# Optimization experiments

Measured on AMD Instinct MI355X. Metric: run time of the kernel, lower is better.

Reference implementation:

```python
import jax, jax.numpy as jnp
import numpy as np

MODEL_DIM = 1024
NUM_HEADS = 16
HEAD_DIM = MODEL_DIM // NUM_HEADS
WINDOW = 4


def local_mask(seq_len):
    i = jnp.arange(seq_len)
    return jnp.abs(i[:, None] - i[None, :]) <= WINDOW  # [S,S] bool


def setup_inputs() -> dict:
    key = jax.random.key(0)
    ks = jax.random.split(key, 9)
    d = MODEL_DIM
    s = 0.02
    return {
        "x": jax.random.normal(ks[0], (4, 2048, d), dtype=jnp.float32),
        "Wq": jax.random.normal(ks[1], (d, d), dtype=jnp.float32) * s,
        "bq": jnp.zeros((d,), dtype=jnp.float32),
        "Wk": jax.random.normal(ks[2], (d, d), dtype=jnp.float32) * s,
        "bk": jnp.zeros((d,), dtype=jnp.float32),
        "Wv": jax.random.normal(ks[3], (d, d), dtype=jnp.float32) * s,
        "bv": jnp.zeros((d,), dtype=jnp.float32),
        "Wo": jax.random.normal(ks[4], (d, d), dtype=jnp.float32) * s,
        "bo": jnp.zeros((d,), dtype=jnp.float32),
    }


def reference(x, Wq, bq, Wk, bk, Wv, bv, Wo, bo):
    B, S, D = x.shape
    H, Hd = NUM_HEADS, HEAD_DIM
    # linear projections (torch Linear: x @ W.T + b; here W stored pre-transposed)
    q = (x @ Wq + bq).reshape(B, S, H, Hd).transpose(0, 2, 1, 3)  # [B,H,S,Hd]
    k = (x @ Wk + bk).reshape(B, S, H, Hd).transpose(0, 2, 1, 3)
    v = (x @ Wv + bv).reshape(B, S, H, Hd).transpose(0, 2, 1, 3)
    scores = jnp.einsum("bhqd,bhkd->bhqk", q, k) / jnp.sqrt(jnp.float32(Hd))
    mask = local_mask(S)[None, None]  # [1,1,S,S]
    scores = jnp.where(mask, scores, -jnp.inf)
    weights = jax.nn.softmax(scores, axis=-1)  # [B,H,S,S]
    out = jnp.einsum("bhqk,bhkd->bhqd", weights, v)
    out = out.transpose(0, 2, 1, 3).reshape(B, S, D)
    out = out @ Wo + bo
    return (out, weights)
```

## Files before the change

kernel.cpp:

```cpp
#include <hip/hip_runtime.h>


typedef __attribute__((ext_vector_type(8))) short short8;
typedef __attribute__((ext_vector_type(4))) float f32x4;

#define B_    4
#define S_    2048
#define D_    1024
#define H_    16
#define HD_   64
#define WIN_  4
#define NROW  (B_ * S_)
#define OUT0_ELEMS  ((size_t)B_ * S_ * D_)
#define TOTAL_CH (67108864ull)
#define Z0_CH 37748736ull
#define Z1_CH 16777216ull
#define ZA_BASE (Z0_CH + Z1_CH)

__device__ __forceinline__ unsigned short f2bf(float f) {
  unsigned int u = __float_as_uint(f);
  u += 0x7fffu + ((u >> 16) & 1u);
  return (unsigned short)(u >> 16);
}
__device__ __forceinline__ float bf2f(unsigned short u) {
  return __uint_as_float(((unsigned int)u) << 16);
}

__device__ __forceinline__ void zstore(f32x4* __restrict__ woutv, size_t g) {
  int row = (int)(g >> 9);
  int f = (int)(g & 511);
  int s = row & (S_ - 1);
  int f0 = (s > WIN_) ? ((s - WIN_) >> 2) : 0;
  int hi = (s + WIN_ < S_ - 1) ? (s + WIN_) : (S_ - 1);
  int f1 = hi >> 2;
  if (f < f0 || f > f1) {
    f32x4 z = {0.f, 0.f, 0.f, 0.f};
    __builtin_nontemporal_store(z, woutv + g);
  }
}

__global__ __launch_bounds__(256) void xconv_k(const float* __restrict__ x,
                                               unsigned short* __restrict__ o) {
  int i = blockIdx.x * 256 + threadIdx.x;
  float4 f = reinterpret_cast<const float4*>(x)[i];
  ushort4 u;
  u.x = f2bf(f.x); u.y = f2bf(f.y); u.z = f2bf(f.z); u.w = f2bf(f.w);
  reinterpret_cast<ushort4*>(o)[i] = u;
}

__global__ __launch_bounds__(256) void wconv_k(const float* __restrict__ W0,
                                               const float* __restrict__ W1,
                                               const float* __restrict__ W2,
                                               const float* __restrict__ W3,
                                               unsigned short* __restrict__ out) {
  __shared__ float t[32][33];
  const float* Ws[4] = {W0, W1, W2, W3};
  const float* W = Ws[blockIdx.z];
  unsigned short* o = out + (size_t)blockIdx.z * D_ * D_;
  int tx = threadIdx.x;
  int ty = threadIdx.y;
  int n0 = blockIdx.x * 32, k0 = blockIdx.y * 32;
#pragma unroll
  for (int i = 0; i < 4; ++i)
    t[ty + 8 * i][tx] = W[(size_t)(k0 + ty + 8 * i) * D_ + (n0 + tx)];
  __syncthreads();
#pragma unroll
  for (int i = 0; i < 4; ++i)
    o[(size_t)(n0 + ty + 8 * i) * D_ + (k0 + tx)] = f2bf(t[tx][ty + 8 * i]);
}

#define GLD16(g, l)                                                            \
  __builtin_amdgcn_global_load_lds(                                            \
      (const __attribute__((address_space(1))) unsigned int*)(g),              \
      (__attribute__((address_space(3))) unsigned int*)(l), 16, 0, 0)

__global__ __launch_bounds__(256) void gemm_qkv_k(
    const unsigned short* __restrict__ A, const unsigned short* __restrict__ Wt,
    const float* __restrict__ bq, const float* __restrict__ bk,
    const float* __restrict__ bv, unsigned short* __restrict__ Qb,
    unsigned short* __restrict__ Kb, unsigned short* __restrict__ Vb,
    float* __restrict__ wout) {
  __shared__ unsigned short As[128 * 32];
  __shared__ unsigned short Bs[128 * 32];
  const int b = blockIdx.x;
  const int g8 = b >> 3, o = b & 7;

  if ((g8 & 3) == 3) {
    const int fb = (g8 >> 2) * 8 + o;
    const unsigned int t0 = fb * 256u + threadIdx.x;
    f32x4* woutv = (f32x4*)wout;
    for (int it = 0; it < 288; ++it)
      zstore(woutv, (size_t)it * 131072u + t0);
    return;
  }

  const int gg = g8 - (g8 >> 2);
  const int row0 = (o * 8 + (gg & 7)) * 128;
  const int col0 = (gg >> 3) * 128;

  const int tid = threadIdx.x;
  const int lane = tid & 63;
  const int wid = tid >> 6;
  const int wm = wid >> 1, wn = wid & 1;

  f32x4 acc[4][4] = {};
  const int frow = lane & 15;
  const int koff = (lane >> 4) << 3;

  for (int kt = 0; kt < 32; ++kt) {
#pragma unroll
    for (int i = 0; i < 2; ++i) {
      int c = tid + (i << 8);
      int r = c >> 2;
      int kk = (c & 3) << 3;
      GLD16(A + (size_t)(row0 + r) * D_ + (kt << 5) + kk, (char*)As + c * 16);
      GLD16(Wt + (size_t)(col0 + r) * D_ + (kt << 5) + kk, (char*)Bs + c * 16);
    }
    __syncthreads();
    short8 af[4], bfr[4];
#pragma unroll
    for (int mi = 0; mi < 4; ++mi)
      af[mi] = *reinterpret_cast<const short8*>(
          &As[(wm * 64 + mi * 16 + frow) * 32 + koff]);
#pragma unroll
    for (int ni = 0; ni < 4; ++ni)
      bfr[ni] = *reinterpret_cast<const short8*>(
          &Bs[(wn * 64 + ni * 16 + frow) * 32 + koff]);
#pragma unroll
    for (int mi = 0; mi < 4; ++mi)
#pragma unroll
      for (int ni = 0; ni < 4; ++ni)
        acc[mi][ni] = __builtin_amdgcn_mfma_f32_16x16x32_bf16(
            af[mi], bfr[ni], acc[mi][ni], 0, 0, 0);
    __syncthreads();
  }

#pragma unroll
  for (int mi = 0; mi < 4; ++mi) {
#pragma unroll
    for (int ni = 0; ni < 4; ++ni) {
#pragma unroll
      for (int r = 0; r < 4; ++r) {
        int gr = row0 + wm * 64 + mi * 16 + ((lane >> 4) << 2) + r;
        int gc = col0 + wn * 64 + ni * 16 + (lane & 15);
        int z = gc >> 10;
        int ci = gc & 1023;
        float bias = (z == 0) ? bq[ci] : (z == 1) ? bk[ci] : bv[ci];
        unsigned short* outp = (z == 0) ? Qb : (z == 1) ? Kb : Vb;
        int bb = gr >> 11, s = gr & (S_ - 1);
        int h = ci >> 6, hd = ci & 63;
        outp[(((size_t)(bb * H_ + h) * S_ + s) << 6) + hd] =
            f2bf(acc[mi][ni][r] + bias);
      }
    }
  }
}

__global__ __launch_bounds__(256) void gemm_out_k(
    const unsigned short* __restrict__ A, const unsigned short* __restrict__ Bt,
    const float* __restrict__ bias, float* __restrict__ o_,
    float* __restrict__ wout) {
  __shared__ unsigned short As[128 * 32];
  __shared__ unsigned short Bs[128 * 32];
  const int b = blockIdx.x;
  const int g8 = b >> 3, o = b & 7;

  if (g8 % 3 == 2) {
    const int fb = (g8 / 3) * 8 + o;
    const unsigned int t0 = fb * 256u + threadIdx.x;
    f32x4* woutv = (f32x4*)wout;
    for (int it = 0; it < 256; ++it)
      zstore(woutv, Z0_CH + (size_t)it * 65536u + t0);
    return;
  }

  const int gg = g8 - (g8 + 1) / 3;
  const int row0 = (o * 8 + (gg & 7)) * 128;
  const int col0 = (gg >> 3) * 128;

  const int tid = threadIdx.x;
  const int lane = tid & 63;
  const int wid = tid >> 6;
  const int wm = wid >> 1, wn = wid & 1;

  f32x4 acc[4][4] = {};
  const int frow = lane & 15;
  const int koff = (lane >> 4) << 3;

  for (int kt = 0; kt < 32; ++kt) {
#pragma unroll
    for (int i = 0; i < 2; ++i) {
      int c = tid + (i << 8);
      int r = c >> 2;
      int kk = (c & 3) << 3;
      GLD16(A + (size_t)(row0 + r) * D_ + (kt << 5) + kk, (char*)As + c * 16);
      GLD16(Bt + (size_t)(col0 + r) * D_ + (kt << 5) + kk, (char*)Bs + c * 16);
    }
    __syncthreads();
    short8 af[4], bfr[4];
#pragma unroll
    for (int mi = 0; mi < 4; ++mi)
      af[mi] = *reinterpret_cast<const short8*>(
          &As[(wm * 64 + mi * 16 + frow) * 32 + koff]);
#pragma unroll
    for (int ni = 0; ni < 4; ++ni)
      bfr[ni] = *reinterpret_cast<const short8*>(
          &Bs[(wn * 64 + ni * 16 + frow) * 32 + koff]);
#pragma unroll
    for (int mi = 0; mi < 4; ++mi)
#pragma unroll
      for (int ni = 0; ni < 4; ++ni)
        acc[mi][ni] = __builtin_amdgcn_mfma_f32_16x16x32_bf16(
            af[mi], bfr[ni], acc[mi][ni], 0, 0, 0);
    __syncthreads();
  }

#pragma unroll
  for (int mi = 0; mi < 4; ++mi) {
#pragma unroll
    for (int ni = 0; ni < 4; ++ni) {
#pragma unroll
      for (int r = 0; r < 4; ++r) {
        int gr = row0 + wm * 64 + mi * 16 + ((lane >> 4) << 2) + r;
        int gc = col0 + wn * 64 + ni * 16 + (lane & 15);
        o_[(size_t)gr * D_ + gc] = acc[mi][ni][r] + bias[gc];
      }
    }
  }
}

__global__ __launch_bounds__(256) void attn_k(const unsigned short* __restrict__ Q,
                                              const unsigned short* __restrict__ K,
                                              const unsigned short* __restrict__ V,
                                              float* __restrict__ wout,
                                              unsigned short* __restrict__ attn) {
  int lane = threadIdx.x & 63;
  int wid = threadIdx.x >> 6;
  int row = blockIdx.x * 4 + wid;
  int s = row & (S_ - 1);
  int bh = row >> 11;
  int b = bh >> 4, h = bh & 15;
  float qd = bf2f(Q[(size_t)row * HD_ + lane]);
  const unsigned short* Kb = K + (size_t)bh * S_ * HD_;
  const unsigned short* Vb = V + (size_t)bh * S_ * HD_;

  float sc[9];
#pragma unroll
  for (int j = 0; j < 9; ++j) {
    int ks = s - WIN_ + j;
    bool ok = (ks >= 0) && (ks < S_);
    float v = ok ? qd * bf2f(Kb[(size_t)ks * HD_ + lane]) : 0.f;
#pragma unroll
    for (int off = 32; off > 0; off >>= 1) v += __shfl_xor(v, off, 64);
    sc[j] = ok ? v * 0.125f : -INFINITY;
  }
  float m = sc[0];
#pragma unroll
  for (int j = 1; j < 9; ++j) m = fmaxf(m, sc[j]);
  float w[9];
  float sum = 0.f;
#pragma unroll
  for (int j = 0; j < 9; ++j) { w[j] = __expf(sc[j] - m); sum += w[j]; }
  float inv = 1.f / sum;
#pragma unroll
  for (int j = 0; j < 9; ++j) w[j] *= inv;

  float o = 0.f;
#pragma unroll
  for (int j = 0; j < 9; ++j) {
    int ks = s - WIN_ + j;
    if (ks >= 0 && ks < S_) o += w[j] * bf2f(Vb[(size_t)ks * HD_ + lane]);
  }
  attn[((size_t)(b * S_ + s)) * D_ + h * HD_ + lane] = f2bf(o);

  const int lo = s - WIN_;
  const int hiq = (s + WIN_ < S_ - 1) ? (s + WIN_) : (S_ - 1);
  const int f0 = (s > WIN_) ? ((s - WIN_) >> 2) : 0;
  const int f1 = hiq >> 2;
  f32x4* rowp = reinterpret_cast<f32x4*>(wout + (size_t)row * S_);
  if (lane <= f1 - f0) {
    f32x4 v4;
#pragma unroll
    for (int e = 0; e < 4; ++e) {
      int d = ((f0 + lane) << 2) + e - lo;
      float val = 0.f;
#pragma unroll
      for (int j = 0; j < 9; ++j)
        if (d == j) val = w[j];
      v4[e] = val;
    }
    __builtin_nontemporal_store(v4, rowp + f0 + lane);
  }

  unsigned int gtid = blockIdx.x * 256u + threadIdx.x;
#pragma unroll
  for (int k2 = 0; k2 < 2; ++k2) {
    size_t g = ZA_BASE + (size_t)k2 * 8388608u + gtid;
    if (g < TOTAL_CH) zstore((f32x4*)wout, g);
  }
}

extern "C" void kernel_launch(void* const* d_in, const int* in_sizes, int n_in,
                              void* d_out, int out_size, void* d_ws,
                              size_t ws_size, hipStream_t stream) {
  const float* x = (const float*)d_in[0];
  const float* Wq = (const float*)d_in[1];
  const float* bq = (const float*)d_in[2];
  const float* Wk = (const float*)d_in[3];
  const float* bk = (const float*)d_in[4];
  const float* Wv = (const float*)d_in[5];
  const float* bv = (const float*)d_in[6];
  const float* Wo = (const float*)d_in[7];
  const float* bo = (const float*)d_in[8];
  float* out = (float*)d_out;
  float* wout = out + OUT0_ELEMS;

  char* ws = (char*)d_ws;
  unsigned short* x_bf = (unsigned short*)(ws);
  unsigned short* Wt = (unsigned short*)(ws + (16ull << 20));
  unsigned short* Qb = (unsigned short*)(ws + (24ull << 20));
  unsigned short* Kb = (unsigned short*)(ws + (40ull << 20));
  unsigned short* Vb = (unsigned short*)(ws + (56ull << 20));
  unsigned short* attn = (unsigned short*)(ws + (72ull << 20));

  xconv_k<<<NROW * D_ / 1024, 256, 0, stream>>>(x, x_bf);
  wconv_k<<<dim3(32, 32, 4), dim3(32, 8), 0, stream>>>(Wq, Wk, Wv, Wo, Wt);
  gemm_qkv_k<<<2048, 256, 0, stream>>>(x_bf, Wt, bq, bk, bv, Qb, Kb, Vb, wout);
  attn_k<<<(B_ * H_ * S_) / 4, 256, 0, stream>>>(Qb, Kb, Vb, wout, attn);
  gemm_out_k<<<768, 256, 0, stream>>>(attn, Wt + (size_t)3 * D_ * D_, bo, out,
                                      wout);
}
```

Measured before the change: 343.2 us.

## Move zero-fill of attention weights from GEMM side-blocks into attention kernel

Removes the extra blocks in the QKV and output GEMMs that zero-filled the 1 GiB weights matrix alongside the GEMM work. The attention kernel now writes each full 2048-wide row itself, with zeros outside the band. This drops the overlap of zero-fill bandwidth with the compute-bound GEMMs and serializes all of it into the attention kernel. It simplifies the block indexing but likely lengthens the attention kernel considerably.

```diff
diff --git a/kernel.cpp b/kernel.cpp
--- a/kernel.cpp
+++ b/kernel.cpp
@@ -12,10 +12,6 @@
 #define WIN_  4
 #define NROW  (B_ * S_)
 #define OUT0_ELEMS  ((size_t)B_ * S_ * D_)
-#define TOTAL_CH (67108864ull)
-#define Z0_CH 37748736ull
-#define Z1_CH 16777216ull
-#define ZA_BASE (Z0_CH + Z1_CH)
 
 __device__ __forceinline__ unsigned short f2bf(float f) {
   unsigned int u = __float_as_uint(f);
@@ -24,19 +20,6 @@
 }
 __device__ __forceinline__ float bf2f(unsigned short u) {
   return __uint_as_float(((unsigned int)u) << 16);
-}
-
-__device__ __forceinline__ void zstore(f32x4* __restrict__ woutv, size_t g) {
-  int row = (int)(g >> 9);
-  int f = (int)(g & 511);
-  int s = row & (S_ - 1);
-  int f0 = (s > WIN_) ? ((s - WIN_) >> 2) : 0;
-  int hi = (s + WIN_ < S_ - 1) ? (s + WIN_) : (S_ - 1);
-  int f1 = hi >> 2;
-  if (f < f0 || f > f1) {
-    f32x4 z = {0.f, 0.f, 0.f, 0.f};
-    __builtin_nontemporal_store(z, woutv + g);
-  }
 }
 
 __global__ __launch_bounds__(256) void xconv_k(const float* __restrict__ x,
@@ -78,23 +61,11 @@
     const unsigned short* __restrict__ A, const unsigned short* __restrict__ Wt,
     const float* __restrict__ bq, const float* __restrict__ bk,
     const float* __restrict__ bv, unsigned short* __restrict__ Qb,
-    unsigned short* __restrict__ Kb, unsigned short* __restrict__ Vb,
-    float* __restrict__ wout) {
+    unsigned short* __restrict__ Kb, unsigned short* __restrict__ Vb) {
   __shared__ unsigned short As[128 * 32];
   __shared__ unsigned short Bs[128 * 32];
-  const int b = blockIdx.x;
-  const int g8 = b >> 3, o = b & 7;
-
-  if ((g8 & 3) == 3) {
-    const int fb = (g8 >> 2) * 8 + o;
-    const unsigned int t0 = fb * 256u + threadIdx.x;
-    f32x4* woutv = (f32x4*)wout;
-    for (int it = 0; it < 288; ++it)
-      zstore(woutv, (size_t)it * 131072u + t0);
-    return;
-  }
-
-  const int gg = g8 - (g8 >> 2);
+  const int g = blockIdx.x;
+  const int o = g & 7, gg = g >> 3;
   const int row0 = (o * 8 + (gg & 7)) * 128;
   const int col0 = (gg >> 3) * 128;
 
@@ -158,23 +129,11 @@
 
 __global__ __launch_bounds__(256) void gemm_out_k(
     const unsigned short* __restrict__ A, const unsigned short* __restrict__ Bt,
-    const float* __restrict__ bias, float* __restrict__ o_,
-    float* __restrict__ wout) {
+    const float* __restrict__ bias, float* __restrict__ o_) {
   __shared__ unsigned short As[128 * 32];
   __shared__ unsigned short Bs[128 * 32];
-  const int b = blockIdx.x;
-  const int g8 = b >> 3, o = b & 7;
-
-  if (g8 % 3 == 2) {
-    const int fb = (g8 / 3) * 8 + o;
-    const unsigned int t0 = fb * 256u + threadIdx.x;
-    f32x4* woutv = (f32x4*)wout;
-    for (int it = 0; it < 256; ++it)
-      zstore(woutv, Z0_CH + (size_t)it * 65536u + t0);
-    return;
-  }
-
-  const int gg = g8 - (g8 + 1) / 3;
+  const int g = blockIdx.x;
+  const int o = g & 7, gg = g >> 3;
   const int row0 = (o * 8 + (gg & 7)) * 128;
   const int col0 = (gg >> 3) * 128;
 
@@ -273,30 +232,26 @@
   }
   attn[((size_t)(b * S_ + s)) * D_ + h * HD_ + lane] = f2bf(o);
 
+  f32x4* rowp = reinterpret_cast<f32x4*>(wout + (size_t)row * S_);
   const int lo = s - WIN_;
-  const int hiq = (s + WIN_ < S_ - 1) ? (s + WIN_) : (S_ - 1);
-  const int f0 = (s > WIN_) ? ((s - WIN_) >> 2) : 0;
-  const int f1 = hiq >> 2;
-  f32x4* rowp = reinterpret_cast<f32x4*>(wout + (size_t)row * S_);
-  if (lane <= f1 - f0) {
-    f32x4 v4;
-#pragma unroll
-    for (int e = 0; e < 4; ++e) {
-      int d = ((f0 + lane) << 2) + e - lo;
-      float val = 0.f;
-#pragma unroll
-      for (int j = 0; j < 9; ++j)
-        if (d == j) val = w[j];
-      v4[e] = val;
-    }
-    __builtin_nontemporal_store(v4, rowp + f0 + lane);
-  }
-
-  unsigned int gtid = blockIdx.x * 256u + threadIdx.x;
-#pragma unroll
-  for (int k2 = 0; k2 < 2; ++k2) {
-    size_t g = ZA_BASE + (size_t)k2 * 8388608u + gtid;
-    if (g < TOTAL_CH) zstore((f32x4*)wout, g);
+  const int hi = s + WIN_;
+#pragma unroll
+  for (int i = 0; i < 8; ++i) {
+    int f = lane + (i << 6);
+    int c0 = f << 2;
+    f32x4 v4 = {0.f, 0.f, 0.f, 0.f};
+    if (c0 + 3 >= lo && c0 <= hi) {
+#pragma unroll
+      for (int e = 0; e < 4; ++e) {
+        int d = c0 + e - lo;
+        float val = 0.f;
+#pragma unroll
+        for (int j = 0; j < 9; ++j)
+          if (d == j) val = w[j];
+        v4[e] = val;
+      }
+    }
+    __builtin_nontemporal_store(v4, rowp + f);
   }
 }
 
@@ -325,8 +280,7 @@
 
   xconv_k<<<NROW * D_ / 1024, 256, 0, stream>>>(x, x_bf);
   wconv_k<<<dim3(32, 32, 4), dim3(32, 8), 0, stream>>>(Wq, Wk, Wv, Wo, Wt);
-  gemm_qkv_k<<<2048, 256, 0, stream>>>(x_bf, Wt, bq, bk, bv, Qb, Kb, Vb, wout);
+  gemm_qkv_k<<<1536, 256, 0, stream>>>(x_bf, Wt, bq, bk, bv, Qb, Kb, Vb);
   attn_k<<<(B_ * H_ * S_) / 4, 256, 0, stream>>>(Qb, Kb, Vb, wout, attn);
-  gemm_out_k<<<768, 256, 0, stream>>>(attn, Wt + (size_t)3 * D_ * D_, bo, out,
-                                      wout);
-}
+  gemm_out_k<<<512, 256, 0, stream>>>(attn, Wt + (size_t)3 * D_ * D_, bo, out);
+}
```

After: 282.6 us. -17.7%, faster.
